# Kernel tuning notes

Measured on AMD Instinct MI355X. Metric: run time of the kernel, lower is better.

The kernel has to match this reference:

```python
import jax, jax.numpy as jnp
import numpy as np

H = 8   # num_key_value_heads
G = 4   # num_query_heads // num_key_value_heads
HQ = H * G  # 32 query heads


def setup_inputs() -> dict:
    key = jax.random.key(0)
    k0, k1, k2, k3 = jax.random.split(key, 4)
    B, N, D = 2, 2048, 2048
    s = 1.0 / np.sqrt(D)
    x = jax.random.normal(k0, (B, N, D), jnp.float32)
    Wq = jax.random.normal(k1, (D, D), jnp.float32) * s
    Wkv = jax.random.normal(k2, (D, 2 * D // G), jnp.float32) * s
    Wp = jax.random.normal(k3, (D, D), jnp.float32) * s
    bp = jnp.zeros((D,), jnp.float32)
    return {"x": x, "Wq": Wq, "Wkv": Wkv, "Wp": Wp, "bp": bp}


def reference(x, Wq, Wkv, Wp, bp):
    B, N, D = x.shape
    C = D // (H * G)  # head dim
    scale = float(np.sqrt(HQ))  # module scales by sqrt(num_query_heads)
    q = (x @ Wq) / scale                     # [B, N, D]
    kv = x @ Wkv                             # [B, N, 2*H*C]
    k, v = jnp.split(kv, 2, axis=-1)         # each [B, N, H*C]
    # q: b n (h g c) -> b g h n c
    q = q.reshape(B, N, H, G, C).transpose(0, 3, 2, 1, 4)
    # k, v: b s (h c) -> b h s c
    k = k.reshape(B, N, H, C).transpose(0, 2, 1, 3)
    v = v.reshape(B, N, H, C).transpose(0, 2, 1, 3)
    sim = jnp.einsum('bghnc,bhsc->bghns', q, k)
    attn = jax.nn.softmax(sim, axis=-1)
    o = jnp.einsum('bghns,bhsc->bghnc', attn, v)
    # b g h n c -> b n (h g c)
    o = o.transpose(0, 3, 2, 1, 4).reshape(B, N, D)
    return o @ Wp + bp
```

## Files before the change

kernel.cpp:

```cpp
#include <hip/hip_runtime.h>
#include <hip/hip_bf16.h>
#include <math.h>

typedef __attribute__((ext_vector_type(8))) __bf16 bf16x8;
typedef __attribute__((ext_vector_type(4))) float f32x4;
typedef __attribute__((ext_vector_type(16))) float f32x16;
typedef __attribute__((ext_vector_type(2))) unsigned u32x2;

#define MFMA16(a, b, c) __builtin_amdgcn_mfma_f32_16x16x32_bf16((a), (b), (c), 0, 0, 0)
#define MFMA32(a, b, c) __builtin_amdgcn_mfma_f32_32x32x16_bf16((a), (b), (c), 0, 0, 0)

#define GLOAD_LDS(g, l)                                                                     \
  __builtin_amdgcn_global_load_lds((const __attribute__((address_space(1))) unsigned int*)(g), \
                                   (__attribute__((address_space(3))) unsigned int*)(l), 16, 0, 0)

static constexpr int Bb  = 2;
static constexpr int Nn  = 2048;
static constexpr int Dd  = 2048;
static constexpr int Hh  = 8;
static constexpr int Gg  = 4;
static constexpr int Cc  = 64;
static constexpr int KVW = 1024;

__device__ __forceinline__ unsigned short f2bf(float f) {
  unsigned int u = __float_as_uint(f);
  u += 0x7FFFu + ((u >> 16) & 1u);
  return (unsigned short)(u >> 16);
}

__global__ void prep(const float* __restrict__ x, unsigned short* __restrict__ xb,
                     const float* __restrict__ Wq, unsigned short* __restrict__ Wqt,
                     const float* __restrict__ Wkv, unsigned short* __restrict__ Wkvt,
                     const float* __restrict__ Wp, unsigned short* __restrict__ Wpt,
                     float qscale) {
  __shared__ float t[32][33];
  int bx = blockIdx.x;
  if (bx < 1024) {
    const int n4 = (Bb * Nn * Dd) / 4;
    int i = bx * 256 + threadIdx.x;
    for (; i < n4; i += 1024 * 256) {
      float4 v = ((const float4*)x)[i];
      ushort4 o;
      o.x = f2bf(v.x); o.y = f2bf(v.y); o.z = f2bf(v.z); o.w = f2bf(v.w);
      ((ushort4*)xb)[i] = o;
    }
    return;
  }
  bx -= 1024;
  const float* W;
  unsigned short* Wt;
  int N, nsh;
  float scale;
  if (bx < 4096) {
    W = Wq; Wt = Wqt; N = Dd; nsh = 6; scale = qscale;
  } else if (bx < 6144) {
    bx -= 4096; W = Wkv; Wt = Wkvt; N = KVW; nsh = 5; scale = 1.0f;
  } else {
    bx -= 6144; W = Wp; Wt = Wpt; N = Dd; nsh = 6; scale = 1.0f;
  }
  const int n0 = (bx & ((1 << nsh) - 1)) * 32;
  const int k0 = (bx >> nsh) * 32;
  for (int i = threadIdx.x; i < 1024; i += blockDim.x) {
    int r = i >> 5, c = i & 31;
    t[r][c] = W[(size_t)(k0 + r) * N + n0 + c];
  }
  __syncthreads();
  for (int i = threadIdx.x; i < 1024; i += blockDim.x) {
    int r = i >> 5, c = i & 31;
    Wt[(size_t)(n0 + r) * Dd + k0 + c] = f2bf(t[c][r] * scale);
  }
}

__global__ void vtrans(const unsigned short* __restrict__ kvb, unsigned short* __restrict__ vT) {
  __shared__ unsigned short t[64][72];
  const int s0 = blockIdx.x * 64;
  const int b = blockIdx.y >> 3, h = blockIdx.y & 7;
  const unsigned short* src = kvb + ((size_t)b * Nn + s0) * KVW + Hh * Cc + h * Cc;
  for (int i = threadIdx.x; i < 4096; i += blockDim.x) {
    int s = i >> 6, c = i & 63;
    t[s][c] = src[(size_t)s * KVW + c];
  }
  __syncthreads();
  unsigned short* dst = vT + (size_t)(b * Hh + h) * Cc * Nn + s0;
  for (int i = threadIdx.x; i < 4096; i += blockDim.x) {
    int c = i >> 6, s = i & 63;
    dst[(size_t)c * Nn + s] = t[s][c];
  }
}

template <int BM, bool OUTF32>
__global__ __launch_bounds__(256, 2)
void gemm_bt(const unsigned short* __restrict__ A, const unsigned short* __restrict__ Bt,
             unsigned short* __restrict__ Cb, float* __restrict__ Cf,
             const float* __restrict__ bias, int M, int N, int K) {
  constexpr int BN = 128;
  constexpr int CA = BM / 8;
  constexpr int CB = BN / 8;
  constexpr int APW = CA / 4, BPW = CB / 4;
  constexpr int MT = BM / 32, NT = BN / 32;
  __shared__ unsigned short As[2][BM * 64];
  __shared__ unsigned short Bs[2][BN * 64];
  const int tid = threadIdx.x;
  const int wid = tid >> 6, lane = tid & 63;
  const size_t m0 = (size_t)blockIdx.x * BM;
  const size_t n0 = (size_t)blockIdx.y * BN;
  const int nk = K >> 6;

  const int sub = lane >> 3, slot = lane & 7;
  const int gslot = slot ^ sub;
  const unsigned short* gA[APW];
  const unsigned short* gB[BPW];
#pragma unroll
  for (int i = 0; i < APW; ++i) {
    const int c = wid * APW + i;
    gA[i] = A + (m0 + c * 8 + sub) * (size_t)K + gslot * 8;
  }
#pragma unroll
  for (int i = 0; i < BPW; ++i) {
    const int c = wid * BPW + i;
    gB[i] = Bt + (n0 + c * 8 + sub) * (size_t)K + gslot * 8;
  }

  auto stage = [&](int bi) {
#pragma unroll
    for (int i = 0; i < APW; ++i) {
      GLOAD_LDS(gA[i], &As[bi][(wid * APW + i) * 512]);
      gA[i] += 64;
    }
#pragma unroll
    for (int i = 0; i < BPW; ++i) {
      GLOAD_LDS(gB[i], &Bs[bi][(wid * BPW + i) * 512]);
      gB[i] += 64;
    }
  };

  const int wr = wid >> 1, wc = wid & 1;
  const int lrow = lane & 15, lg = lane >> 4;
  int aoff[MT][2], boff[NT][2];
#pragma unroll
  for (int mt = 0; mt < MT; ++mt)
#pragma unroll
    for (int kc = 0; kc < 2; ++kc) {
      const int sl = (((kc << 2) + lg) ^ (lrow & 7)) << 4;
      aoff[mt][kc] = (wr * (BM / 2) + mt * 16 + lrow) * 128 + sl;
    }
#pragma unroll
  for (int nt = 0; nt < NT; ++nt)
#pragma unroll
    for (int kc = 0; kc < 2; ++kc) {
      const int sl = (((kc << 2) + lg) ^ (lrow & 7)) << 4;
      boff[nt][kc] = (wc * (BN / 2) + nt * 16 + lrow) * 128 + sl;
    }

  const f32x4 zero = {0.f, 0.f, 0.f, 0.f};
  f32x4 acc[MT][NT];
#pragma unroll
  for (int i = 0; i < MT; ++i)
#pragma unroll
    for (int j = 0; j < NT; ++j) acc[i][j] = zero;

  auto compute = [&](int bi) {
    const char* Ab = (const char*)&As[bi][0];
    const char* Bb2 = (const char*)&Bs[bi][0];
#pragma unroll
    for (int kc = 0; kc < 2; ++kc) {
      bf16x8 af[MT], bfr[NT];
#pragma unroll
      for (int mt = 0; mt < MT; ++mt) af[mt] = *(const bf16x8*)(Ab + aoff[mt][kc]);
#pragma unroll
      for (int nt = 0; nt < NT; ++nt) bfr[nt] = *(const bf16x8*)(Bb2 + boff[nt][kc]);
#pragma unroll
      for (int mt = 0; mt < MT; ++mt)
#pragma unroll
        for (int nt = 0; nt < NT; ++nt) acc[mt][nt] = MFMA16(af[mt], bfr[nt], acc[mt][nt]);
    }
  };

  stage(0);
  __syncthreads();
  for (int kt = 0; kt < nk; kt += 2) {
    stage(1);
    compute(0);
    __syncthreads();
    if (kt + 2 < nk) stage(0);
    compute(1);
    __syncthreads();
  }

#pragma unroll
  for (int mt = 0; mt < MT; ++mt)
#pragma unroll
    for (int nt = 0; nt < NT; ++nt) {
      const size_t col = n0 + wc * (BN / 2) + nt * 16 + lrow;
#pragma unroll
      for (int i = 0; i < 4; ++i) {
        const size_t r = m0 + wr * (BM / 2) + mt * 16 + lg * 4 + i;
        if constexpr (OUTF32)
          Cf[r * N + col] = acc[mt][nt][i] + bias[col];
        else
          Cb[r * N + col] = f2bf(acc[mt][nt][i]);
      }
    }
}

__global__ __launch_bounds__(512, 4)
void attn_kernel(const unsigned short* __restrict__ qb, const unsigned short* __restrict__ kvb,
                 const unsigned short* __restrict__ vT, unsigned short* __restrict__ ob) {
  __shared__ unsigned short Ks[2][4096];
  __shared__ unsigned short Vs[2][4096];
  const int tid = threadIdx.x;
  const int wid = tid >> 6, lane = tid & 63;
  const int r31 = lane & 31, hi = lane >> 5, r7 = r31 & 7;
  const int q0 = blockIdx.x * 256 + wid * 32;
  const int bhg = blockIdx.y;
  const int b = bhg >> 5, h = (bhg >> 2) & 7, g = bhg & 3;

  const unsigned short* kptr = kvb + (size_t)b * Nn * KVW + h * Cc;
  const unsigned short* vptr = vT + (size_t)(b * Hh + h) * Cc * Nn;

  const int sub = lane >> 3, slot = lane & 7;
  const int gslot = slot ^ sub;
  const unsigned short* gk = kptr + (size_t)(wid * 8 + sub) * KVW + gslot * 8;
  const unsigned short* gv = vptr + (size_t)(wid * 8 + sub) * Nn + gslot * 8;

  bf16x8 qf[4];
  {
    const unsigned short* qrow =
        qb + ((size_t)b * Nn + q0 + r31) * Dd + h * (Gg * Cc) + g * Cc + hi * 8;
#pragma unroll
    for (int ks = 0; ks < 4; ++ks) qf[ks] = *(const bf16x8*)(qrow + ks * 16);
  }

  union { unsigned u[4]; bf16x8 v; } ones;
  ones.u[0] = ones.u[1] = ones.u[2] = ones.u[3] = 0x3F803F80u;

  int off[4];
#pragma unroll
  for (int ks = 0; ks < 4; ++ks) off[ks] = r31 * 128 + (((2 * ks + hi) ^ r7) << 4);

  f32x16 O0 = (f32x16)0.0f, O1 = (f32x16)0.0f, Lacc = (f32x16)0.0f;

  auto stage = [&](int bi) {
    GLOAD_LDS(gk, &Ks[bi][wid * 512]);
    GLOAD_LDS(gv, &Vs[bi][wid * 512]);
    gk += (size_t)64 * KVW;
    gv += 64;
  };

  auto compute = [&](const unsigned short* Kb_, const unsigned short* Vb_) {
    const char* Kb = (const char*)Kb_;
    const char* Vb = (const char*)Vb_;
    f32x16 S0 = (f32x16)0.0f, S1 = (f32x16)0.0f;
    __builtin_amdgcn_s_setprio(1);
#pragma unroll
    for (int ks = 0; ks < 4; ++ks) {
      bf16x8 k0 = *(const bf16x8*)(Kb + off[ks]);
      bf16x8 k1 = *(const bf16x8*)(Kb + off[ks] + 4096);
      S0 = MFMA32(k0, qf[ks], S0);
      S1 = MFMA32(k1, qf[ks], S1);
    }
    __builtin_amdgcn_s_setprio(0);
    unsigned pk[16];
#pragma unroll
    for (int kt2 = 0; kt2 < 2; ++kt2)
#pragma unroll
      for (int blk = 0; blk < 4; ++blk)
#pragma unroll
        for (int m = 0; m < 2; ++m) {
          float pa = __expf(kt2 ? S1[4 * blk + 2 * m] : S0[4 * blk + 2 * m]);
          float pb = __expf(kt2 ? S1[4 * blk + 2 * m + 1] : S0[4 * blk + 2 * m + 1]);
          pk[kt2 * 8 + blk * 2 + m] = __builtin_amdgcn_perm(
              __float_as_uint(pb), __float_as_uint(pa), 0x07060302u);
        }
    __builtin_amdgcn_s_setprio(1);
#pragma unroll
    for (int vs = 0; vs < 4; ++vs) {
      const int base = (vs >> 1) * 8 + (vs & 1) * 4;
      u32x2 rA = __builtin_amdgcn_permlane32_swap(pk[base + 0], pk[base + 2], false, false);
      u32x2 rB = __builtin_amdgcn_permlane32_swap(pk[base + 1], pk[base + 3], false, false);
      union { unsigned u[4]; bf16x8 v; } pf;
      pf.u[0] = rA.x; pf.u[1] = rB.x; pf.u[2] = rA.y; pf.u[3] = rB.y;
      bf16x8 v0 = *(const bf16x8*)(Vb + off[vs]);
      bf16x8 v1 = *(const bf16x8*)(Vb + off[vs] + 4096);
      O0 = MFMA32(pf.v, v0, O0);
      O1 = MFMA32(pf.v, v1, O1);
      Lacc = MFMA32(pf.v, ones.v, Lacc);
    }
    __builtin_amdgcn_s_setprio(0);
  };

  stage(0);
  __syncthreads();
  for (int t = 0; t < Nn / 64; t += 2) {
    stage(1);
    compute(Ks[0], Vs[0]);
    __syncthreads();
    if (t + 2 < Nn / 64) stage(0);
    compute(Ks[1], Vs[1]);
    __syncthreads();
  }

  const size_t orow_base = (size_t)b * Nn + q0;
  const int ocol = h * (Gg * Cc) + g * Cc;
#pragma unroll
  for (int r = 0; r < 16; ++r) {
    const int q_r = (r & 3) + 8 * (r >> 2) + 4 * hi;
    const float li = 1.0f / Lacc[r];
    const size_t basep = (orow_base + q_r) * Dd + ocol;
    ob[basep + r31] = f2bf(O0[r] * li);
    ob[basep + 32 + r31] = f2bf(O1[r] * li);
  }
}

extern "C" void kernel_launch(void* const* d_in, const int* in_sizes, int n_in,
                              void* d_out, int out_size, void* d_ws, size_t ws_size,
                              hipStream_t stream) {
  const float* x   = (const float*)d_in[0];
  const float* Wq  = (const float*)d_in[1];
  const float* Wkv = (const float*)d_in[2];
  const float* Wp  = (const float*)d_in[3];
  const float* bp  = (const float*)d_in[4];
  float* out = (float*)d_out;

  char* ws = (char*)d_ws;
  size_t off = 0;
  auto alloc = [&](size_t bytes) {
    char* p = ws + off;
    off += (bytes + 255) & ~(size_t)255;
    return p;
  };
  unsigned short* xb   = (unsigned short*)alloc((size_t)Bb * Nn * Dd * 2);
  unsigned short* Wqt  = (unsigned short*)alloc((size_t)Dd * Dd * 2);
  unsigned short* Wkvt = (unsigned short*)alloc((size_t)KVW * Dd * 2);
  unsigned short* Wpt  = (unsigned short*)alloc((size_t)Dd * Dd * 2);
  unsigned short* qbf  = (unsigned short*)alloc((size_t)Bb * Nn * Dd * 2);
  unsigned short* kvb  = (unsigned short*)alloc((size_t)Bb * Nn * KVW * 2);
  unsigned short* vT   = (unsigned short*)alloc((size_t)Bb * Hh * Cc * Nn * 2);
  unsigned short* ob   = xb;

  const int M = Bb * Nn;
  const float qscale = 0.17677669529663687f;

  prep<<<11264, 256, 0, stream>>>(x, xb, Wq, Wqt, Wkv, Wkvt, Wp, Wpt, qscale);

  gemm_bt<128, false><<<dim3(M / 128, Dd / 128), 256, 0, stream>>>(xb, Wqt, qbf, nullptr, nullptr, M, Dd, Dd);
  gemm_bt<64, false><<<dim3(M / 64, KVW / 128), 256, 0, stream>>>(xb, Wkvt, kvb, nullptr, nullptr, M, KVW, Dd);
  vtrans<<<dim3(Nn / 64, Bb * Hh), 256, 0, stream>>>(kvb, vT);
  attn_kernel<<<dim3(Nn / 256, Bb * Hh * Gg), 512, 0, stream>>>(qbf, kvb, vT, ob);
  gemm_bt<128, true><<<dim3(M / 128, Dd / 128), 256, 0, stream>>>(ob, Wpt, nullptr, out, bp, M, Dd, Dd);
}
```

Measured before the change: 216.0 us.

## Fuse V transpose into KV GEMM epilogue and use exp2 with folded log2e

```diff
diff --git a/kernel.cpp b/kernel.cpp
--- a/kernel.cpp
+++ b/kernel.cpp
@@ -27,6 +27,12 @@
   u += 0x7FFFu + ((u >> 16) & 1u);
   return (unsigned short)(u >> 16);
 }
+
+#if __has_builtin(__builtin_amdgcn_exp2f)
+__device__ __forceinline__ float fexp2(float x) { return __builtin_amdgcn_exp2f(x); }
+#else
+__device__ __forceinline__ float fexp2(float x) { return __expf(x * 0.6931471805599453f); }
+#endif
 
 __global__ void prep(const float* __restrict__ x, unsigned short* __restrict__ xb,
                      const float* __restrict__ Wq, unsigned short* __restrict__ Wqt,
@@ -71,28 +77,12 @@
   }
 }
 
-__global__ void vtrans(const unsigned short* __restrict__ kvb, unsigned short* __restrict__ vT) {
-  __shared__ unsigned short t[64][72];
-  const int s0 = blockIdx.x * 64;
-  const int b = blockIdx.y >> 3, h = blockIdx.y & 7;
-  const unsigned short* src = kvb + ((size_t)b * Nn + s0) * KVW + Hh * Cc + h * Cc;
-  for (int i = threadIdx.x; i < 4096; i += blockDim.x) {
-    int s = i >> 6, c = i & 63;
-    t[s][c] = src[(size_t)s * KVW + c];
-  }
-  __syncthreads();
-  unsigned short* dst = vT + (size_t)(b * Hh + h) * Cc * Nn + s0;
-  for (int i = threadIdx.x; i < 4096; i += blockDim.x) {
-    int c = i >> 6, s = i & 63;
-    dst[(size_t)c * Nn + s] = t[s][c];
-  }
-}
-
-template <int BM, bool OUTF32>
+template <int BM, bool OUTF32, bool VOUT = false>
 __global__ __launch_bounds__(256, 2)
 void gemm_bt(const unsigned short* __restrict__ A, const unsigned short* __restrict__ Bt,
              unsigned short* __restrict__ Cb, float* __restrict__ Cf,
-             const float* __restrict__ bias, int M, int N, int K) {
+             const float* __restrict__ bias, unsigned short* __restrict__ vTo,
+             int M, int N, int K) {
   constexpr int BN = 128;
   constexpr int CA = BM / 8;
   constexpr int CB = BN / 8;
@@ -187,6 +177,26 @@
     __syncthreads();
   }
 
+  if (VOUT && n0 >= 512) {
+#pragma unroll
+    for (int mt = 0; mt < MT; ++mt)
+#pragma unroll
+      for (int nt = 0; nt < NT; ++nt) {
+        const int colv = (int)(n0 - 512) + wc * (BN / 2) + nt * 16 + lrow;
+        const int h = colv >> 6, c = colv & 63;
+        const size_t r0 = m0 + wr * (BM / 2) + mt * 16 + lg * 4;
+        const int b = (int)(r0 >> 11);
+        const int s = (int)(r0 & 2047);
+        ushort4 o;
+        o.x = f2bf(acc[mt][nt][0]);
+        o.y = f2bf(acc[mt][nt][1]);
+        o.z = f2bf(acc[mt][nt][2]);
+        o.w = f2bf(acc[mt][nt][3]);
+        *(ushort4*)&vTo[(((size_t)b * Hh + h) * Cc + c) * (size_t)Nn + s] = o;
+      }
+    return;
+  }
+
 #pragma unroll
   for (int mt = 0; mt < MT; ++mt)
 #pragma unroll
@@ -267,8 +277,8 @@
       for (int blk = 0; blk < 4; ++blk)
 #pragma unroll
         for (int m = 0; m < 2; ++m) {
-          float pa = __expf(kt2 ? S1[4 * blk + 2 * m] : S0[4 * blk + 2 * m]);
-          float pb = __expf(kt2 ? S1[4 * blk + 2 * m + 1] : S0[4 * blk + 2 * m + 1]);
+          float pa = fexp2(kt2 ? S1[4 * blk + 2 * m] : S0[4 * blk + 2 * m]);
+          float pb = fexp2(kt2 ? S1[4 * blk + 2 * m + 1] : S0[4 * blk + 2 * m + 1]);
           pk[kt2 * 8 + blk * 2 + m] = __builtin_amdgcn_perm(
               __float_as_uint(pb), __float_as_uint(pa), 0x07060302u);
         }
@@ -339,13 +349,15 @@
   unsigned short* ob   = xb;
 
   const int M = Bb * Nn;
-  const float qscale = 0.17677669529663687f;
+  const float qscale = 0.17677669529663687f * 1.4426950408889634f;
 
   prep<<<11264, 256, 0, stream>>>(x, xb, Wq, Wqt, Wkv, Wkvt, Wp, Wpt, qscale);
 
-  gemm_bt<128, false><<<dim3(M / 128, Dd / 128), 256, 0, stream>>>(xb, Wqt, qbf, nullptr, nullptr, M, Dd, Dd);
-  gemm_bt<64, false><<<dim3(M / 64, KVW / 128), 256, 0, stream>>>(xb, Wkvt, kvb, nullptr, nullptr, M, KVW, Dd);
-  vtrans<<<dim3(Nn / 64, Bb * Hh), 256, 0, stream>>>(kvb, vT);
+  gemm_bt<128, false><<<dim3(M / 128, Dd / 128), 256, 0, stream>>>(
+      xb, Wqt, qbf, nullptr, nullptr, nullptr, M, Dd, Dd);
+  gemm_bt<64, false, true><<<dim3(M / 64, KVW / 128), 256, 0, stream>>>(
+      xb, Wkvt, kvb, nullptr, nullptr, vT, M, KVW, Dd);
   attn_kernel<<<dim3(Nn / 256, Bb * Hh * Gg), 512, 0, stream>>>(qbf, kvb, vT, ob);
-  gemm_bt<128, true><<<dim3(M / 128, Dd / 128), 256, 0, stream>>>(ob, Wpt, nullptr, out, bp, M, Dd, Dd);
-}
+  gemm_bt<128, true><<<dim3(M / 128, Dd / 128), 256, 0, stream>>>(
+      ob, Wpt, nullptr, out, bp, nullptr, M, Dd, Dd);
+}
```

Measured after the change: 209.3 us. 1.03x faster.
